# Optimization experiments

Measured on AMD Instinct MI355X. Metric: run time of the kernel, lower is better.

Reference implementation:

```python
import jax, jax.numpy as jnp
import numpy as np

M = 10000          # reservoir size
EMBED = 768        # ViT-base embed dim
L = 12             # ViT-base blocks
B = 16             # batch
NUM_CLASSES = 200
P = 0.5            # bernoulli keep prob (1-p in torch.full(1-p))
C3 = 1e-6
LN_EPS = 1e-5
LEAK = 0.01


def setup_inputs() -> dict:
    key = jax.random.key(0)
    k1, k2, k3, k4 = jax.random.split(key, 4)
    fs = jax.random.normal(k1, (L, B, EMBED), dtype=jnp.float32)
    Win = jax.random.normal(k2, (EMBED, M), dtype=jnp.float32)
    scale = 100.0 / (P * M)
    Wres = (jax.random.uniform(k3, (M, M), dtype=jnp.float32) < (1.0 - P)).astype(jnp.float32) * scale
    Wout = jax.random.normal(k4, (M, NUM_CLASSES), dtype=jnp.float32) * 0.01
    return {"fs": fs, "Win": Win, "Wres": Wres, "Wout": Wout}


def reference(fs, Win, Wres, Wout):
    # fs: [L, B, EMBED] CLS-token features per ViT block
    a_coef = 2.0 * C3 * (1.0 - P) * np.float32(np.sqrt(M))

    def step(h, f):
        f_in = f @ Win                                   # [B, M]
        a = a_coef * jnp.sum(jnp.abs(h))                  # scalar
        h_new = f_in + h @ Wres.T - a                     # sparse.mm(Wres, h.T).T == h @ Wres.T
        # F.layer_norm(h, h.size()): normalize over ALL elements (B and M)
        mu = jnp.mean(h_new)
        var = jnp.mean(jnp.square(h_new - mu))
        h_norm = (h_new - mu) * jax.lax.rsqrt(var + LN_EPS)
        h_out = jnp.where(h_norm >= 0, h_norm, LEAK * h_norm)  # leaky_relu
        return h_out, None

    h0 = jnp.zeros((fs.shape[1], M), dtype=fs.dtype)
    h, _ = jax.lax.scan(step, h0, fs)
    return h @ Wout
```

## Files before the change

kernel.cpp:

```cpp
#include <hip/hip_runtime.h>
#include <hip/hip_bf16.h>


typedef short short8 __attribute__((ext_vector_type(8)));
typedef float f32x4 __attribute__((ext_vector_type(4)));
typedef unsigned int u32x4 __attribute__((ext_vector_type(4)));

#define NB 16
#define MR 10000
#define KCOL 10240
#define IPAD 10112
#define BMROW 1280
#define NELEM 160000.0f
#define NFIN 480

__device__ __forceinline__ void block_reduce_add2(float s, float q, float* slot) {
  #pragma unroll
  for (int d = 32; d > 0; d >>= 1) {
    s += __shfl_down(s, d, 64);
    q += __shfl_down(q, d, 64);
  }
  __shared__ float ls[8], lq[8];
  int w = threadIdx.x >> 6;
  if ((threadIdx.x & 63) == 0) { ls[w] = s; lq[w] = q; }
  __syncthreads();
  if (threadIdx.x == 0) {
    float S = 0.f, Q = 0.f;
    int nw = blockDim.x >> 6;
    for (int k = 0; k < nw; ++k) { S += ls[k]; Q += lq[k]; }
    atomicAdd(&slot[0], S);
    atomicAdd(&slot[1], Q);
  }
}

__global__ __launch_bounds__(256) void k_front(const float* __restrict__ Wres,
                                               const float* __restrict__ fs,
                                               const float* __restrict__ Win,
                                               unsigned char* __restrict__ bm,
                                               float* __restrict__ fin,
                                               float* __restrict__ slots) {
  int bx = blockIdx.x;
  int tid = threadIdx.x;
  if (bx < NFIN) {
    int xcd = bx & 7, s = bx >> 3;
    int t = s % 12, cb = xcd * 5 + s / 12;
    int i0 = cb * 256 + tid;
    float* dst = fin + (size_t)t * (NB * KCOL) + i0;
    float acc[NB];
    #pragma unroll
    for (int b = 0; b < NB; ++b) acc[b] = 0.f;
    bool pad = (i0 >= MR);
    if (pad) {
      #pragma unroll
      for (int b = 0; b < NB; ++b) dst[b * KCOL] = 0.f;
    } else {
      const float* fsr = fs + t * (NB * 768);
      #pragma unroll 4
      for (int k = 0; k < 768; ++k) {
        float w = Win[(size_t)k * MR + i0];
        #pragma unroll
        for (int b = 0; b < NB; ++b) acc[b] += fsr[b * 768 + k] * w;
      }
      #pragma unroll
      for (int b = 0; b < NB; ++b) dst[b * KCOL] = acc[b];
    }
    if (t == 0) {
      float sm = 0.f, sq = 0.f;
      if (!pad) {
        #pragma unroll
        for (int b = 0; b < NB; ++b) { sm += acc[b]; sq += acc[b] * acc[b]; }
      }
      block_reduce_add2(sm, sq, slots);
    }
    return;
  }
  int i = bx - NFIN;
  #pragma unroll
  for (int m = 0; m < 5; ++m) {
    int jb = tid + 256 * m;
    unsigned int b = 0;
    if (i < MR && jb < 1250) {
      const float* src = Wres + (size_t)i * MR + jb * 8;
      float4 v0 = *(const float4*)(src);
      float4 v1 = *(const float4*)(src + 4);
      b  = (v0.x != 0.f ? 1u : 0u);
      b |= (v0.y != 0.f ? 2u : 0u);
      b |= (v0.z != 0.f ? 4u : 0u);
      b |= (v0.w != 0.f ? 8u : 0u);
      b |= (v1.x != 0.f ? 16u : 0u);
      b |= (v1.y != 0.f ? 32u : 0u);
      b |= (v1.z != 0.f ? 64u : 0u);
      b |= (v1.w != 0.f ? 128u : 0u);
    }
    int phys = ((jb >> 6) << 6) | ((jb & 3) << 4) | ((jb >> 2) & 15);
    bm[(size_t)i * BMROW + phys] = (unsigned char)b;
  }
}

__device__ __forceinline__ unsigned int pair_bf16(unsigned int w, int bit) {
  unsigned int t = (w << (30 - bit)) >> 30;
  unsigned int m, u;
  asm("v_mul_u32_u24 %0, 0x8001, %1" : "=v"(m) : "v"(t));
  m &= 0x00010001u;
  asm("v_mul_u32_u24 %0, 0x3f80, %1" : "=v"(u) : "v"(m));
  return u;
}
__device__ __forceinline__ short8 expand8(unsigned int w, int bitbase) {
  union { unsigned int u[4]; short8 s; } r;
  #pragma unroll
  for (int p = 0; p < 4; ++p) r.u[p] = pair_bf16(w, bitbase + 2 * p);
  return r.s;
}

__global__ __launch_bounds__(256) void k_gemm(const float* __restrict__ hsrc,
                                              const float* __restrict__ slot,
                                              const unsigned char* __restrict__ bm,
                                              float* __restrict__ part) {
  __shared__ unsigned int Alds[16 * 644];
  int n = blockIdx.x;
  int id = (n & 7) * 79 + (n >> 3);
  int ib = id >> 3, ksp = id & 7;
  int tid = threadIdx.x;
  float mu = slot[0] * (1.f / NELEM);
  float var = slot[1] * (1.f / NELEM) - mu * mu;
  float rs = rsqrtf(var + 1e-5f);
  float murs = mu * rs;
  {
    int row = tid >> 4, jj = tid & 15;
    const float* hrow = hsrc + row * KCOL + ksp * 1280;
    unsigned int* lrow = Alds + row * 644;
    #pragma unroll 4
    for (int it = 0; it < 40; ++it) {
      int jp = jj + 16 * it;
      float2 v = *(const float2*)(hrow + 2 * jp);
      float x0 = fmaf(v.x, rs, -murs); x0 = (x0 >= 0.f) ? x0 : 0.01f * x0;
      float x1 = fmaf(v.y, rs, -murs); x1 = (x1 >= 0.f) ? x1 : 0.01f * x1;
      unsigned int pk;
      asm("v_cvt_pk_bf16_f32 %0, %1, %2" : "=v"(pk) : "v"(x0), "v"(x1));
      lrow[jp] = pk;
    }
  }
  __syncthreads();
  int wave = tid >> 6, lane = tid & 63;
  int r = lane & 15, q = lane >> 4;
  int i0 = ib * 128 + wave * 32;
  const unsigned int* ab = Alds + r * 644 + q * 4;
  const unsigned char* b0p = bm + (size_t)(i0 + r) * BMROW;
  f32x4 acc0 = {0.f, 0.f, 0.f, 0.f}, acc1 = {0.f, 0.f, 0.f, 0.f};
  for (int g = 0; g < 5; ++g) {
    int sg = 5 * ksp + g;
    int off = ((sg >> 1) << 6) + (q << 4) + ((sg & 1) << 3);
    uint2 w0 = *(const uint2*)(b0p + off);
    uint2 w1 = *(const uint2*)(b0p + 16 * BMROW + off);
    #pragma unroll
    for (int e8 = 0; e8 < 8; ++e8) {
      int ksl = g * 8 + e8;
      union { u32x4 v; short8 s; } a;
      a.v = *(const u32x4*)(ab + ksl * 16);
      unsigned int wb0 = (e8 < 4) ? w0.x : w0.y;
      unsigned int wb1 = (e8 < 4) ? w1.x : w1.y;
      int bb = (e8 & 3) * 8;
      acc0 = __builtin_amdgcn_mfma_f32_16x16x32_bf16(a.s, expand8(wb0, bb), acc0, 0, 0, 0);
      acc1 = __builtin_amdgcn_mfma_f32_16x16x32_bf16(a.s, expand8(wb1, bb), acc1, 0, 0, 0);
    }
  }
  float* pp = part + (size_t)ksp * (NB * IPAD) + (q * 4) * IPAD + i0 + r;
  #pragma unroll
  for (int rg = 0; rg < 4; ++rg) {
    pp[rg * IPAD] = acc0[rg];
    pp[rg * IPAD + 16] = acc1[rg];
  }
}

__global__ __launch_bounds__(256) void k_finish(const float* __restrict__ part,
                                                float* __restrict__ finio,
                                                float* __restrict__ slot) {
  int u = blockIdx.x * 256 + threadIdx.x;
  float s = 0.f, q = 0.f;
  if (u < 40000) {
    int b = u / 2500, i = (u % 2500) * 4;
    size_t o = (size_t)b * IPAD + i;
    float4 p = *(const float4*)(part + o);
    #pragma unroll
    for (int sp = 1; sp < 8; ++sp) {
      float4 t = *(const float4*)(part + (size_t)sp * (NB * IPAD) + o);
      p.x += t.x; p.y += t.y; p.z += t.z; p.w += t.w;
    }
    float* fp = finio + (size_t)b * KCOL + i;
    float4 f = *(const float4*)(fp);
    float4 h;
    h.x = fmaf(0.02f, p.x, f.x);
    h.y = fmaf(0.02f, p.y, f.y);
    h.z = fmaf(0.02f, p.z, f.z);
    h.w = fmaf(0.02f, p.w, f.w);
    *(float4*)(fp) = h;
    s = h.x + h.y + h.z + h.w;
    q = h.x * h.x + h.y * h.y + h.z * h.z + h.w * h.w;
  }
  block_reduce_add2(s, q, slot);
}

__global__ __launch_bounds__(256) void k_classify(const float* __restrict__ hraw,
                                                  const float* __restrict__ slot,
                                                  const float* __restrict__ Wout,
                                                  float* __restrict__ out) {
  int cg = blockIdx.x % 25, ksp = blockIdx.x / 25;
  int tid = threadIdx.x;
  int kp = tid >> 3, cl = tid & 7;
  int c = cg * 8 + cl;
  int kbase = ksp * 1280;
  int kend = min(kbase + 1280, MR);
  float mu = slot[0] * (1.f / NELEM);
  float var = slot[1] * (1.f / NELEM) - mu * mu;
  float rs = rsqrtf(var + 1e-5f);
  float murs = mu * rs;
  float acc[NB];
  #pragma unroll
  for (int b = 0; b < NB; ++b) acc[b] = 0.f;
  for (int k = kbase + kp; k < kend; k += 32) {
    float w = Wout[(size_t)k * 200 + c];
    #pragma unroll
    for (int b = 0; b < NB; ++b) {
      float x = fmaf(hraw[(size_t)b * KCOL + k], rs, -murs);
      x = (x >= 0.f) ? x : 0.01f * x;
      acc[b] = fmaf(x, w, acc[b]);
    }
  }
  #pragma unroll
  for (int d = 8; d < 64; d <<= 1) {
    #pragma unroll
    for (int b = 0; b < NB; ++b) acc[b] += __shfl_down(acc[b], d, 64);
  }
  __shared__ float lds[4 * 128];
  int w = tid >> 6, lane = tid & 63;
  if (lane < 8) {
    #pragma unroll
    for (int b = 0; b < NB; ++b) lds[w * 128 + lane * 16 + b] = acc[b];
  }
  __syncthreads();
  if (tid < 128) {
    int clx = tid >> 4, b = tid & 15;
    float S = lds[clx * 16 + b] + lds[128 + clx * 16 + b] +
              lds[256 + clx * 16 + b] + lds[384 + clx * 16 + b];
    atomicAdd(&out[b * 200 + cg * 8 + clx], S);
  }
}

extern "C" void kernel_launch(void* const* d_in, const int* in_sizes, int n_in,
                              void* d_out, int out_size, void* d_ws, size_t ws_size,
                              hipStream_t stream) {
  const float* fs   = (const float*)d_in[0];
  const float* Win  = (const float*)d_in[1];
  const float* Wres = (const float*)d_in[2];
  const float* Wout = (const float*)d_in[3];
  float* out = (float*)d_out;
  char* ws = (char*)d_ws;

  size_t off_bm   = 256;
  size_t off_fin  = off_bm + (size_t)IPAD * BMROW;
  size_t off_part = off_fin + (size_t)12 * NB * KCOL * 4;
  size_t need     = off_part + (size_t)8 * NB * IPAD * 4;
  if (ws_size < need) return;

  float* slots = (float*)ws;
  unsigned char* bm = (unsigned char*)(ws + off_bm);
  float* fin = (float*)(ws + off_fin);
  float* part = (float*)(ws + off_part);

  hipMemsetAsync(slots, 0, 256, stream);
  hipMemsetAsync(out, 0, (size_t)NB * 200 * sizeof(float), stream);

  k_front<<<NFIN + IPAD, 256, 0, stream>>>(Wres, fs, Win, bm, fin, slots);

  for (int t = 1; t < 12; ++t) {
    k_gemm<<<632, 256, 0, stream>>>(fin + (size_t)(t - 1) * NB * KCOL,
                                    slots + 2 * (t - 1), bm, part);
    k_finish<<<157, 256, 0, stream>>>(part, fin + (size_t)t * NB * KCOL,
                                      slots + 2 * t);
  }
  k_classify<<<200, 256, 0, stream>>>(fin + (size_t)11 * NB * KCOL,
                                      slots + 22, Wout, out);
}
```

Measured before the change: 925.5 us.

## Fuse split-K reduction into GEMM via last-block atomic counter

Merges the separate finish kernel into the recurrent GEMM kernel. The last of the eight split-K blocks for each row tile, detected with a per-tile atomic counter, sums the partials, updates the state and accumulates the layer-norm statistics. It also folds the output zeroing into the front kernel and uses a single memset. This removes 11 kernel launches and their dependency gaps, at the cost of threadfence and atomic overhead and a serialized tail done by the last block of each tile.

```diff
diff --git a/kernel.cpp b/kernel.cpp
--- a/kernel.cpp
+++ b/kernel.cpp
@@ -38,9 +38,14 @@
                                                const float* __restrict__ Win,
                                                unsigned char* __restrict__ bm,
                                                float* __restrict__ fin,
-                                               float* __restrict__ slots) {
+                                               float* __restrict__ slots,
+                                               float* __restrict__ out) {
   int bx = blockIdx.x;
   int tid = threadIdx.x;
+  if (bx == NFIN + IPAD) {
+    for (int c = tid; c < NB * 200; c += 256) out[c] = 0.f;
+    return;
+  }
   if (bx < NFIN) {
     int xcd = bx & 7, s = bx >> 3;
     int t = s % 12, cb = xcd * 5 + s / 12;
@@ -112,17 +117,20 @@
   return r.s;
 }
 
-__global__ __launch_bounds__(256) void k_gemm(const float* __restrict__ hsrc,
-                                              const float* __restrict__ slot,
+__global__ __launch_bounds__(256) void k_step(const float* __restrict__ hsrc,
+                                              float* __restrict__ finio,
+                                              const float* __restrict__ slotp,
+                                              float* __restrict__ slotn,
                                               const unsigned char* __restrict__ bm,
-                                              float* __restrict__ part) {
+                                              float* __restrict__ part,
+                                              int* __restrict__ cntt) {
   __shared__ unsigned int Alds[16 * 644];
   int n = blockIdx.x;
   int id = (n & 7) * 79 + (n >> 3);
   int ib = id >> 3, ksp = id & 7;
   int tid = threadIdx.x;
-  float mu = slot[0] * (1.f / NELEM);
-  float var = slot[1] * (1.f / NELEM) - mu * mu;
+  float mu = slotp[0] * (1.f / NELEM);
+  float var = slotp[1] * (1.f / NELEM) - mu * mu;
   float rs = rsqrtf(var + 1e-5f);
   float murs = mu * rs;
   {
@@ -143,9 +151,9 @@
   __syncthreads();
   int wave = tid >> 6, lane = tid & 63;
   int r = lane & 15, q = lane >> 4;
-  int i0 = ib * 128 + wave * 32;
+  int i0w = ib * 128 + wave * 32;
   const unsigned int* ab = Alds + r * 644 + q * 4;
-  const unsigned char* b0p = bm + (size_t)(i0 + r) * BMROW;
+  const unsigned char* b0p = bm + (size_t)(i0w + r) * BMROW;
   f32x4 acc0 = {0.f, 0.f, 0.f, 0.f}, acc1 = {0.f, 0.f, 0.f, 0.f};
   for (int g = 0; g < 5; ++g) {
     int sg = 5 * ksp + g;
@@ -164,40 +172,38 @@
       acc1 = __builtin_amdgcn_mfma_f32_16x16x32_bf16(a.s, expand8(wb1, bb), acc1, 0, 0, 0);
     }
   }
-  float* pp = part + (size_t)ksp * (NB * IPAD) + (q * 4) * IPAD + i0 + r;
+  float* pp = part + (size_t)ksp * (NB * IPAD) + (q * 4) * IPAD + i0w + r;
   #pragma unroll
   for (int rg = 0; rg < 4; ++rg) {
     pp[rg * IPAD] = acc0[rg];
     pp[rg * IPAD + 16] = acc1[rg];
   }
-}
-
-__global__ __launch_bounds__(256) void k_finish(const float* __restrict__ part,
-                                                float* __restrict__ finio,
-                                                float* __restrict__ slot) {
-  int u = blockIdx.x * 256 + threadIdx.x;
-  float s = 0.f, q = 0.f;
-  if (u < 40000) {
-    int b = u / 2500, i = (u % 2500) * 4;
-    size_t o = (size_t)b * IPAD + i;
-    float4 p = *(const float4*)(part + o);
-    #pragma unroll
-    for (int sp = 1; sp < 8; ++sp) {
-      float4 t = *(const float4*)(part + (size_t)sp * (NB * IPAD) + o);
-      p.x += t.x; p.y += t.y; p.z += t.z; p.w += t.w;
-    }
-    float* fp = finio + (size_t)b * KCOL + i;
-    float4 f = *(const float4*)(fp);
-    float4 h;
-    h.x = fmaf(0.02f, p.x, f.x);
-    h.y = fmaf(0.02f, p.y, f.y);
-    h.z = fmaf(0.02f, p.z, f.z);
-    h.w = fmaf(0.02f, p.w, f.w);
-    *(float4*)(fp) = h;
-    s = h.x + h.y + h.z + h.w;
-    q = h.x * h.x + h.y * h.y + h.z * h.z + h.w * h.w;
-  }
-  block_reduce_add2(s, q, slot);
+  __threadfence();
+  __syncthreads();
+  __shared__ int lastf;
+  if (tid == 0) {
+    int old = atomicAdd(&cntt[ib], 1);
+    lastf = (old == 7);
+  }
+  __syncthreads();
+  if (!lastf) return;
+  __builtin_amdgcn_fence(__ATOMIC_ACQUIRE, "agent");
+  int i0 = ib * 128;
+  int iloc = tid & 127, bh = tid >> 7;
+  float sm = 0.f, sq = 0.f;
+  #pragma unroll
+  for (int rep = 0; rep < 8; ++rep) {
+    int b = bh * 8 + rep;
+    size_t o = (size_t)b * IPAD + i0 + iloc;
+    float v = part[o];
+    #pragma unroll
+    for (int sp = 1; sp < 8; ++sp) v += part[(size_t)sp * (NB * IPAD) + o];
+    float* fp = finio + (size_t)b * KCOL + i0 + iloc;
+    float h = fmaf(0.02f, v, *fp);
+    *fp = h;
+    if (i0 + iloc < MR) { sm += h; sq += h * h; }
+  }
+  block_reduce_add2(sm, sq, slotn);
 }
 
 __global__ __launch_bounds__(256) void k_classify(const float* __restrict__ hraw,
@@ -256,27 +262,28 @@
   float* out = (float*)d_out;
   char* ws = (char*)d_ws;
 
-  size_t off_bm   = 256;
+  size_t off_cnt  = 128;
+  size_t off_bm   = 4096;
   size_t off_fin  = off_bm + (size_t)IPAD * BMROW;
   size_t off_part = off_fin + (size_t)12 * NB * KCOL * 4;
   size_t need     = off_part + (size_t)8 * NB * IPAD * 4;
   if (ws_size < need) return;
 
   float* slots = (float*)ws;
+  int* cnt = (int*)(ws + off_cnt);
   unsigned char* bm = (unsigned char*)(ws + off_bm);
   float* fin = (float*)(ws + off_fin);
   float* part = (float*)(ws + off_part);
 
-  hipMemsetAsync(slots, 0, 256, stream);
-  hipMemsetAsync(out, 0, (size_t)NB * 200 * sizeof(float), stream);
-
-  k_front<<<NFIN + IPAD, 256, 0, stream>>>(Wres, fs, Win, bm, fin, slots);
+  hipMemsetAsync(ws, 0, 4096, stream);
+
+  k_front<<<NFIN + IPAD + 1, 256, 0, stream>>>(Wres, fs, Win, bm, fin, slots, out);
 
   for (int t = 1; t < 12; ++t) {
-    k_gemm<<<632, 256, 0, stream>>>(fin + (size_t)(t - 1) * NB * KCOL,
-                                    slots + 2 * (t - 1), bm, part);
-    k_finish<<<157, 256, 0, stream>>>(part, fin + (size_t)t * NB * KCOL,
-                                      slots + 2 * t);
+    k_step<<<632, 256, 0, stream>>>(fin + (size_t)(t - 1) * NB * KCOL,
+                                    fin + (size_t)t * NB * KCOL,
+                                    slots + 2 * (t - 1), slots + 2 * t,
+                                    bm, part, cnt + 79 * (t - 1));
   }
   k_classify<<<200, 256, 0, stream>>>(fin + (size_t)11 * NB * KCOL,
                                       slots + 22, Wout, out);
```

Result: slower. 1.591 ms (+71.9%).
